# Optimization experiments

Measured on AMD Instinct MI355X. Metric: run time of the kernel, lower is better.

## Reference

```python
import jax, jax.numpy as jnp
import numpy as np

N_EMBD = 1024
N_HEAD = 16
HEAD_DIM = N_EMBD // N_HEAD
B, S = 4, 1024


def setup_inputs() -> dict:
    key = jax.random.key(0)
    k1, k2, k3 = jax.random.split(key, 3)
    scale = 0.02
    return {
        "x": jax.random.normal(k1, (B, S, N_EMBD), dtype=jnp.float32),
        "Wqkv": jax.random.normal(k2, (N_EMBD, 3 * N_EMBD), dtype=jnp.float32) * scale,
        "bqkv": jnp.zeros((3 * N_EMBD,), dtype=jnp.float32),
        "Wproj": jax.random.normal(k3, (N_EMBD, N_EMBD), dtype=jnp.float32) * scale,
        "bproj": jnp.zeros((N_EMBD,), dtype=jnp.float32),
    }


def reference(x, Wqkv, bqkv, Wproj, bproj):
    b, s, e = x.shape
    qkv = x @ Wqkv + bqkv  # (b, s, 3e)
    q, k, v = jnp.split(qkv, 3, axis=-1)
    # (b, h, s, d)
    q = q.reshape(b, s, N_HEAD, HEAD_DIM).transpose(0, 2, 1, 3)
    k = k.reshape(b, s, N_HEAD, HEAD_DIM).transpose(0, 2, 1, 3)
    v = v.reshape(b, s, N_HEAD, HEAD_DIM).transpose(0, 2, 1, 3)
    scores = jnp.einsum("bhqd,bhkd->bhqk", q, k) / jnp.sqrt(
        jnp.asarray(HEAD_DIM, dtype=x.dtype)
    )
    causal = jnp.tril(jnp.ones((s, s), dtype=bool))  # (s, s)
    scores = jnp.where(causal[None, None, :, :], scores, jnp.asarray(-jnp.inf, dtype=scores.dtype))
    attn = jax.nn.softmax(scores, axis=-1)
    out = jnp.einsum("bhqk,bhkd->bhqd", attn, v)
    out = out.transpose(0, 2, 1, 3).reshape(b, s, e)
    return out @ Wproj + bproj
```

## Files before the change

kernel.cpp:

```cpp
#include <hip/hip_runtime.h>

#define S_LEN 1024
#define EMB   1024
#define NH    16
#define HD    64
#define BATCH 4
#define M_TOT 4096
#define QSZ   (BATCH * NH * S_LEN * HD)

typedef __attribute__((ext_vector_type(4))) float  f32x4;
typedef __attribute__((ext_vector_type(8))) __bf16 bf16x8;

__device__ __forceinline__ unsigned short f2bf(float f) {
  union { float f; unsigned u; } a; a.f = f;
  unsigned r = a.u + 0x7fffu + ((a.u >> 16) & 1u);
  return (unsigned short)(r >> 16);
}

__device__ __forceinline__ float fexp2(float x) {
#if __has_builtin(__builtin_amdgcn_exp2f)
  return __builtin_amdgcn_exp2f(x);
#else
  return exp2f(x);
#endif
}

__global__ void cvt_bf16(const float4* __restrict__ in, ushort4* __restrict__ out, int n4) {
  int i = blockIdx.x * blockDim.x + threadIdx.x;
  if (i >= n4) return;
  float4 v = in[i];
  ushort4 o;
  o.x = f2bf(v.x); o.y = f2bf(v.y); o.z = f2bf(v.z); o.w = f2bf(v.w);
  out[i] = o;
}

__global__ void cvt_transpose(const float* __restrict__ in, unsigned short* __restrict__ out,
                              int K, int N) {
  __shared__ unsigned short tile[32][33];
  int n0 = blockIdx.x * 32, k0 = blockIdx.y * 32;
  int tx = threadIdx.x, ty = threadIdx.y;
  #pragma unroll
  for (int r = ty; r < 32; r += 8)
    tile[r][tx] = f2bf(in[(size_t)(k0 + r) * N + n0 + tx]);
  __syncthreads();
  #pragma unroll
  for (int r = ty; r < 32; r += 8)
    out[(size_t)(n0 + r) * K + k0 + tx] = tile[tx][r];
}

template<int EPI>
__global__ __launch_bounds__(256) void gemm_bt(
    const unsigned short* __restrict__ A,
    const unsigned short* __restrict__ Bt,
    const float* __restrict__ bias,
    void* __restrict__ outp,
    int M, int N, int K)
{
  __shared__ alignas(16) char smem[49152];
  unsigned short* As = (unsigned short*)smem;
  unsigned short* Bs = (unsigned short*)(smem + 24576);
  const int m0 = blockIdx.x * 128, n0 = blockIdx.y * 128;
  const int t = threadIdx.x;
  const int wid = t >> 6, lane = t & 63;
  const int wr = wid >> 1, wc = wid & 1;
  const int lr = lane & 15, lg = lane >> 4;
  const int nkt = K >> 5;

  f32x4 acc[4][4] = {};

  auto STAGE = [&](int b, int kt) {
    const int k0 = kt << 5;
    #pragma unroll
    for (int c = 0; c < 2; ++c) {
      int idx8 = (c * 4 + wid) * 64 + lane;
      int row  = idx8 >> 2, col = (idx8 & 3) << 3;
      const unsigned short* gA = A  + (size_t)(m0 + row) * K + k0 + col;
      const unsigned short* gB = Bt + (size_t)(n0 + row) * K + k0 + col;
      __builtin_amdgcn_global_load_lds(
          (const __attribute__((address_space(1))) unsigned int*)gA,
          (__attribute__((address_space(3))) unsigned int*)(As + b * 4096 + (c * 4 + wid) * 512),
          16, 0, 0);
      __builtin_amdgcn_global_load_lds(
          (const __attribute__((address_space(1))) unsigned int*)gB,
          (__attribute__((address_space(3))) unsigned int*)(Bs + b * 4096 + (c * 4 + wid) * 512),
          16, 0, 0);
    }
  };

  STAGE(0, 0);
  STAGE(1, 1);

  for (int kt = 0; kt < nkt; ++kt) {
    if (kt + 2 < nkt) {
      STAGE((kt + 2) % 3, kt + 2);
      asm volatile("s_waitcnt vmcnt(8)" ::: "memory");
    } else if (kt + 1 < nkt) {
      asm volatile("s_waitcnt vmcnt(4)" ::: "memory");
    } else {
      asm volatile("s_waitcnt vmcnt(0)" ::: "memory");
    }
    __builtin_amdgcn_s_barrier();
    asm volatile("" ::: "memory");

    const unsigned short* Ab = As + (kt % 3) * 4096;
    const unsigned short* Bb = Bs + (kt % 3) * 4096;
    bf16x8 af[4], bfr[4];
    #pragma unroll
    for (int i = 0; i < 4; ++i)
      af[i] = *(const bf16x8*)(Ab + (wr * 64 + i * 16 + lr) * 32 + lg * 8);
    #pragma unroll
    for (int j = 0; j < 4; ++j)
      bfr[j] = *(const bf16x8*)(Bb + (wc * 64 + j * 16 + lr) * 32 + lg * 8);
    __builtin_amdgcn_s_setprio(1);
    #pragma unroll
    for (int i = 0; i < 4; ++i)
      #pragma unroll
      for (int j = 0; j < 4; ++j)
        acc[i][j] = __builtin_amdgcn_mfma_f32_16x16x32_bf16(af[i], bfr[j], acc[i][j], 0, 0, 0);
    __builtin_amdgcn_s_setprio(0);

    asm volatile("s_waitcnt lgkmcnt(0)" ::: "memory");
    __builtin_amdgcn_s_barrier();
  }

  if (EPI == 0) {
    unsigned short* O = (unsigned short*)outp;
    const int sec = n0 >> 10;
    if (sec < 2) {
      #pragma unroll
      for (int i = 0; i < 4; ++i)
        #pragma unroll
        for (int j = 0; j < 4; ++j) {
          const int col = n0 + wc * 64 + j * 16 + lr;
          const float bv = bias[col];
          const int cc = col & 1023, h = cc >> 6, d = cc & 63;
          #pragma unroll
          for (int r = 0; r < 4; ++r) {
            const int row = m0 + wr * 64 + i * 16 + lg * 4 + r;
            float v = acc[i][j][r] + bv;
            if (sec == 0) v *= 0.18033688f;
            const int bb = row >> 10, ss = row & 1023;
            size_t off = (size_t)sec * QSZ +
                         (((size_t)(bb * NH + h) * S_LEN + ss) * HD + d);
            O[off] = f2bf(v);
          }
        }
    } else {
      unsigned short* T = (unsigned short*)smem;
      __syncthreads();
      #pragma unroll
      for (int i = 0; i < 4; ++i)
        #pragma unroll
        for (int j = 0; j < 4; ++j) {
          const int ci = wc * 64 + j * 16 + lr;
          const float bv = bias[n0 + ci];
          union { ushort4 s4; __bf16 b[4]; } pk;
          #pragma unroll
          for (int r = 0; r < 4; ++r) pk.b[r] = (__bf16)(acc[i][j][r] + bv);
          *(ushort4*)(T + ci * 136 + wr * 64 + i * 16 + lg * 4) = pk.s4;
        }
      __syncthreads();
      const int ci = t >> 1;
      const int cc = (n0 - 2048) + ci;
      const int h = cc >> 6, d = cc & 63;
      const int bb = m0 >> 10, s0 = m0 & 1023;
      unsigned short* dst = O + 2ull * QSZ +
          ((size_t)(bb * NH + h) * HD + d) * S_LEN + s0;
      #pragma unroll
      for (int q = 0; q < 8; ++q) {
        const int spos = (t & 1) * 8 + q;
        bf16x8 vv = *(const bf16x8*)(T + ci * 136 + spos * 8);
        *(bf16x8*)(dst + spos * 8) = vv;
      }
    }
  } else {
    #pragma unroll
    for (int i = 0; i < 4; ++i)
      #pragma unroll
      for (int j = 0; j < 4; ++j) {
        const int col = n0 + wc * 64 + j * 16 + lr;
        const float bv = bias[col];
        #pragma unroll
        for (int r = 0; r < 4; ++r) {
          const int row = m0 + wr * 64 + i * 16 + lg * 4 + r;
          ((float*)outp)[(size_t)row * (size_t)N + col] = acc[i][j][r] + bv;
        }
      }
  }
}

__device__ __forceinline__ void group_tile(
    const bf16x8 (&kf)[8], const bf16x8 (&vf)[8], const bf16x8 (&qf)[2],
    int kt, int q0, bool diag, int lr, int lg,
    float& m, float& lp, f32x4 (&o)[4])
{
  f32x4 sacc[4] = {};
  __builtin_amdgcn_s_setprio(1);
  #pragma unroll
  for (int nt = 0; nt < 4; ++nt)
    #pragma unroll
    for (int kk = 0; kk < 2; ++kk)
      sacc[nt] = __builtin_amdgcn_mfma_f32_16x16x32_bf16(kf[nt * 2 + kk], qf[kk], sacc[nt], 0, 0, 0);
  __builtin_amdgcn_s_setprio(0);

  float p[16];
  if (diag) {
    const int q = q0 + lr;
    #pragma unroll
    for (int nt = 0; nt < 4; ++nt)
      #pragma unroll
      for (int r = 0; r < 4; ++r) {
        int k = kt * 64 + nt * 16 + lg * 4 + r;
        p[nt * 4 + r] = (k > q) ? -1e30f : sacc[nt][r];
      }
  } else {
    #pragma unroll
    for (int nt = 0; nt < 4; ++nt)
      #pragma unroll
      for (int r = 0; r < 4; ++r)
        p[nt * 4 + r] = sacc[nt][r];
  }

  float r8[8], r4[4];
  #pragma unroll
  for (int i = 0; i < 8; ++i) r8[i] = fmaxf(p[i], p[i + 8]);
  #pragma unroll
  for (int i = 0; i < 4; ++i) r4[i] = fmaxf(r8[i], r8[i + 4]);
  float pm = fmaxf(fmaxf(r4[0], r4[1]), fmaxf(r4[2], r4[3]));
  if (__any(pm > m + 11.5f)) {
    float px = fmaxf(pm, __shfl_xor(pm, 16, 64));
    px = fmaxf(px, __shfl_xor(px, 32, 64));
    float mn = fmaxf(m, px);
    float fs = fexp2(m - mn);
    lp *= fs;
    #pragma unroll
    for (int dt = 0; dt < 4; ++dt)
      #pragma unroll
      for (int r = 0; r < 4; ++r) o[dt][r] *= fs;
    m = mn;
  }
  #pragma unroll
  for (int i = 0; i < 16; ++i) p[i] = fexp2(p[i] - m);

  float s8[8], s4[4];
  #pragma unroll
  for (int i = 0; i < 8; ++i) s8[i] = p[i] + p[i + 8];
  #pragma unroll
  for (int i = 0; i < 4; ++i) s4[i] = s8[i] + s8[i + 4];
  lp += (s4[0] + s4[1]) + (s4[2] + s4[3]);

  union { unsigned u[8]; __bf16 b[16]; } W;
  #pragma unroll
  for (int i = 0; i < 16; ++i) W.b[i] = (__bf16)p[i];

  const int dl0 = ((2 * (lg & 1) + (lg >> 1)) * 16 + lr) << 2;
  const int dl1 = ((2 * ((lg & 1) ^ 1) + (lg >> 1)) * 16 + lr) << 2;
  const bool oddlg = (lg & 1) != 0;
  const bool hb    = (lg >> 1) != 0;
  union { unsigned u[4]; bf16x8 v; } T0, T1;
  #pragma unroll
  for (int kk = 0; kk < 2; ++kk) {
    #pragma unroll
    for (int c = 0; c < 2; ++c) {
      unsigned vlo = W.u[4 * kk + c];
      unsigned vhi = W.u[4 * kk + 2 + c];
      unsigned s0 = oddlg ? vhi : vlo;
      unsigned s1 = oddlg ? vlo : vhi;
      unsigned r0 = (unsigned)__builtin_amdgcn_ds_permute(dl0, (int)s0);
      unsigned r1 = (unsigned)__builtin_amdgcn_ds_permute(dl1, (int)s1);
      unsigned* T = kk ? T1.u : T0.u;
      T[c]     = hb ? r1 : r0;
      T[2 + c] = hb ? r0 : r1;
    }
  }

  __builtin_amdgcn_s_setprio(1);
  #pragma unroll
  for (int dt = 0; dt < 4; ++dt) {
    o[dt] = __builtin_amdgcn_mfma_f32_16x16x32_bf16(vf[dt * 2 + 0], T0.v, o[dt], 0, 0, 0);
    o[dt] = __builtin_amdgcn_mfma_f32_16x16x32_bf16(vf[dt * 2 + 1], T1.v, o[dt], 0, 0, 0);
  }
  __builtin_amdgcn_s_setprio(0);
}

__device__ __forceinline__ void group_epilogue(
    const f32x4 (&o)[4], float lp, int q0, int lr, int lg,
    char* Ep, unsigned short* __restrict__ attout, int bb, int h)
{
  float l2 = lp + __shfl_xor(lp, 16, 64);
  float l4 = l2 + __shfl_xor(l2, 32, 64);
  float rl = 1.0f / l4;
  #pragma unroll
  for (int dt = 0; dt < 4; ++dt) {
    union { ushort4 s4; __bf16 b[4]; } ov;
    #pragma unroll
    for (int r = 0; r < 4; ++r) ov.b[r] = (__bf16)(o[dt][r] * rl);
    int byt = (lr * 128 + (dt * 16 + lg * 4) * 2) ^ ((lr & 7) << 4);
    *(ushort4*)(Ep + byt) = ov.s4;
  }
  asm volatile("s_waitcnt lgkmcnt(0)" ::: "memory");
  const int lane = lr + lg * 16;
  const int ql = lane >> 2, c = lane & 3;
  #pragma unroll
  for (int s = 0; s < 2; ++s) {
    int byt = (ql * 128 + (c * 16 + s * 8) * 2) ^ ((ql & 7) << 4);
    bf16x8 vrow = *(const bf16x8*)(Ep + byt);
    *(bf16x8*)(attout + (size_t)(bb * S_LEN + q0 + ql) * EMB + h * HD + c * 16 + s * 8) = vrow;
  }
}

__global__ __launch_bounds__(256, 2) void attn_fwd(
    const unsigned short* __restrict__ Q,
    const unsigned short* __restrict__ K,
    const unsigned short* __restrict__ Vt,
    unsigned short* __restrict__ attout)
{
  __shared__ alignas(16) char stage[2][16384];
  __shared__ alignas(16) char Ep_lds[4][2048];
  const int bid = blockIdx.x;
  const int bh   = ((bid & 7) << 3) | ((bid >> 3) & 7);
  const int base = bid >> 6;
  const int wv = threadIdx.x >> 6, lane = threadIdx.x & 63;
  const int pi = base * 4 + wv;
  const int lr = lane & 15, lg = lane >> 4;
  const int nkt  = 16 - base;
  const int nktl = base + 1;
  const int q0h = (63 - pi) * 16, q0l = pi * 16;
  const unsigned short* Qb = Q  + (size_t)bh * (S_LEN * HD);
  const unsigned short* Kh = K  + (size_t)bh * (S_LEN * HD);
  const unsigned short* Vh = Vt + (size_t)bh * (HD * S_LEN);
  const int bb = bh >> 4, h = bh & 15;

  auto STAGE = [&](int b, int kt) {
    char* lb = &stage[b][0];
    #pragma unroll
    for (int j = 0; j < 4; ++j) {
      if (wv < 2) {
        int L = wv * 4096 + j * 1024 + lane * 16;
        int row = L >> 7, c = (L >> 4) & 7;
        const unsigned short* src = Kh + (size_t)(kt * 64 + row) * HD + ((c ^ (row & 7)) << 3);
        __builtin_amdgcn_global_load_lds(
            (const __attribute__((address_space(1))) unsigned int*)src,
            (__attribute__((address_space(3))) unsigned int*)(lb + wv * 4096 + j * 1024),
            16, 0, 0);
      } else {
        int L = (wv - 2) * 4096 + j * 1024 + lane * 16;
        int row = L >> 7, c = (L >> 4) & 7;
        const unsigned short* src = Vh + (size_t)row * S_LEN + kt * 64 + ((c ^ (row & 7)) << 3);
        __builtin_amdgcn_global_load_lds(
            (const __attribute__((address_space(1))) unsigned int*)src,
            (__attribute__((address_space(3))) unsigned int*)(lb + 8192 + (wv - 2) * 4096 + j * 1024),
            16, 0, 0);
      }
    }
  };

  bf16x8 qfh[2], qfl[2];
  #pragma unroll
  for (int kk = 0; kk < 2; ++kk) {
    qfh[kk] = *(const bf16x8*)(Qb + (size_t)(q0h + lr) * HD + kk * 32 + lg * 8);
    qfl[kk] = *(const bf16x8*)(Qb + (size_t)(q0l + lr) * HD + kk * 32 + lg * 8);
  }

  float mh = -1e30f, lph = 0.f, ml = -1e30f, lpl = 0.f;
  f32x4 oh[4] = {}, ol[4] = {};

  STAGE(0, 0);
  asm volatile("s_waitcnt vmcnt(0)" ::: "memory");
  __syncthreads();

  for (int kt = 0; kt < nkt; ++kt) {
    const int cur = kt & 1;
    if (kt + 1 < nkt) STAGE(cur ^ 1, kt + 1);

    const char* sb = &stage[cur][0];
    bf16x8 kf[8], vf[8];
    #pragma unroll
    for (int nt = 0; nt < 4; ++nt)
      #pragma unroll
      for (int kk = 0; kk < 2; ++kk) {
        const int byt = (nt * 16 + lr) * 128 + ((((kk << 2) + lg) ^ (lr & 7)) << 4);
        kf[nt * 2 + kk] = *(const bf16x8*)(sb + byt);
        vf[nt * 2 + kk] = *(const bf16x8*)(sb + 8192 + byt);
      }

    group_tile(kf, vf, qfh, kt, q0h, kt == nkt - 1, lr, lg, mh, lph, oh);
    if (kt < nktl)
      group_tile(kf, vf, qfl, kt, q0l, kt == nktl - 1, lr, lg, ml, lpl, ol);

    asm volatile("s_waitcnt vmcnt(0)" ::: "memory");
    __syncthreads();
  }

  char* Ep = &Ep_lds[wv][0];
  group_epilogue(oh, lph, q0h, lr, lg, Ep, attout, bb, h);
  group_epilogue(ol, lpl, q0l, lr, lg, Ep, attout, bb, h);
}

extern "C" void kernel_launch(void* const* d_in, const int* in_sizes, int n_in,
                              void* d_out, int out_size, void* d_ws, size_t ws_size,
                              hipStream_t stream) {
  const float* x     = (const float*)d_in[0];
  const float* Wqkv  = (const float*)d_in[1];
  const float* bqkv  = (const float*)d_in[2];
  const float* Wproj = (const float*)d_in[3];
  const float* bproj = (const float*)d_in[4];

  unsigned short* xb     = (unsigned short*)d_ws;
  unsigned short* WqkvT  = xb     + (size_t)M_TOT * EMB;
  unsigned short* WprojT = WqkvT  + (size_t)3 * EMB * EMB;
  unsigned short* qkv    = WprojT + (size_t)EMB * EMB;
  unsigned short* att    = qkv    + 3ull * QSZ;

  cvt_bf16<<<dim3((M_TOT * EMB / 4 + 255) / 256), dim3(256), 0, stream>>>(
      (const float4*)x, (ushort4*)xb, M_TOT * EMB / 4);
  cvt_transpose<<<dim3(3 * EMB / 32, EMB / 32), dim3(32, 8), 0, stream>>>(Wqkv, WqkvT, EMB, 3 * EMB);
  cvt_transpose<<<dim3(EMB / 32, EMB / 32), dim3(32, 8), 0, stream>>>(Wproj, WprojT, EMB, EMB);

  gemm_bt<0><<<dim3(M_TOT / 128, 3 * EMB / 128), dim3(256), 0, stream>>>(
      xb, WqkvT, bqkv, (void*)qkv, M_TOT, 3 * EMB, EMB);

  attn_fwd<<<dim3(8 * BATCH * NH), dim3(256), 0, stream>>>(
      qkv, qkv + QSZ, qkv + 2ull * QSZ, att);

  gemm_bt<1><<<dim3(M_TOT / 128, EMB / 128), dim3(256), 0, stream>>>(
      att, WprojT, bproj, d_out, M_TOT, EMB, EMB);
}
```

Baseline: 99.92 us.

## Add 256x256-tile QKV GEMM with direct-to-LDS loads and swizzled shared memory

Replaces the generic 128x128 templated GEMM for the QKV projection with a dedicated 256x256-tile kernel. It uses 512 threads, a K step of 64, global_load_lds transfers straight into double-buffered LDS, and an XOR swizzle to avoid bank conflicts. The V-transpose epilogue is redone in four quadrant passes through shared memory. The aim is more operand reuse per block and cheaper staging, at the cost of only 192 blocks on the grid (fewer than the CU count) and 128 KB of LDS per block. The projection GEMM keeps the old design as a non-templated kernel.

```diff
diff --git a/kernel.cpp b/kernel.cpp
--- a/kernel.cpp
+++ b/kernel.cpp
@@ -48,12 +48,145 @@
     out[(size_t)(n0 + r) * K + k0 + tx] = tile[tx][r];
 }
 
-template<int EPI>
-__global__ __launch_bounds__(256) void gemm_bt(
+__global__ __launch_bounds__(512, 2) void gemm_qkv256(
     const unsigned short* __restrict__ A,
     const unsigned short* __restrict__ Bt,
     const float* __restrict__ bias,
-    void* __restrict__ outp,
+    unsigned short* __restrict__ O)
+{
+  __shared__ alignas(16) char smem[131072];
+  const int m0 = blockIdx.x * 256, n0 = blockIdx.y * 256;
+  const int K = EMB;
+  const int t = threadIdx.x;
+  const int wid = t >> 6, lane = t & 63;
+  const int wm = wid >> 2, wn = wid & 3;
+  const int lr = lane & 15, lg = lane >> 4;
+  const int nkt = K >> 6;
+
+  f32x4 acc[8][4] = {};
+
+  auto STAGE = [&](int b, int kt) {
+    const int k0 = kt << 6;
+    #pragma unroll
+    for (int l = 0; l < 4; ++l) {
+      const int L = l * 8192 + t * 16;
+      const int row = L >> 7;
+      const int c = (L >> 4) & 7;
+      const int ce = ((c ^ (row & 7)) << 3);
+      const unsigned short* gA = A  + (size_t)(m0 + row) * K + k0 + ce;
+      const unsigned short* gB = Bt + (size_t)(n0 + row) * K + k0 + ce;
+      __builtin_amdgcn_global_load_lds(
+          (const __attribute__((address_space(1))) unsigned int*)gA,
+          (__attribute__((address_space(3))) unsigned int*)(smem + b * 32768 + L),
+          16, 0, 0);
+      __builtin_amdgcn_global_load_lds(
+          (const __attribute__((address_space(1))) unsigned int*)gB,
+          (__attribute__((address_space(3))) unsigned int*)(smem + 65536 + b * 32768 + L),
+          16, 0, 0);
+    }
+  };
+
+  STAGE(0, 0);
+
+  for (int kt = 0; kt < nkt; ++kt) {
+    const int cur = kt & 1;
+    if (kt + 1 < nkt) {
+      STAGE(cur ^ 1, kt + 1);
+      asm volatile("s_waitcnt vmcnt(8)" ::: "memory");
+    } else {
+      asm volatile("s_waitcnt vmcnt(0)" ::: "memory");
+    }
+    __builtin_amdgcn_s_barrier();
+    asm volatile("" ::: "memory");
+
+    const char* Ab = smem + cur * 32768;
+    const char* Bb = smem + 65536 + cur * 32768;
+    #pragma unroll
+    for (int s = 0; s < 2; ++s) {
+      bf16x8 af[8], bfr[4];
+      #pragma unroll
+      for (int i = 0; i < 8; ++i) {
+        const int row = wm * 128 + i * 16 + lr;
+        const int byt = row * 128 + (((s * 4 + lg) ^ (row & 7)) << 4);
+        af[i] = *(const bf16x8*)(Ab + byt);
+      }
+      #pragma unroll
+      for (int j = 0; j < 4; ++j) {
+        const int row = wn * 64 + j * 16 + lr;
+        const int byt = row * 128 + (((s * 4 + lg) ^ (row & 7)) << 4);
+        bfr[j] = *(const bf16x8*)(Bb + byt);
+      }
+      __builtin_amdgcn_s_setprio(1);
+      #pragma unroll
+      for (int i = 0; i < 8; ++i)
+        #pragma unroll
+        for (int j = 0; j < 4; ++j)
+          acc[i][j] = __builtin_amdgcn_mfma_f32_16x16x32_bf16(af[i], bfr[j], acc[i][j], 0, 0, 0);
+      __builtin_amdgcn_s_setprio(0);
+    }
+    asm volatile("s_waitcnt lgkmcnt(0)" ::: "memory");
+    __builtin_amdgcn_s_barrier();
+  }
+
+  const int sec = n0 >> 10;
+  if (sec < 2) {
+    #pragma unroll
+    for (int i = 0; i < 8; ++i)
+      #pragma unroll
+      for (int j = 0; j < 4; ++j) {
+        const int col = n0 + wn * 64 + j * 16 + lr;
+        const float bv = bias[col];
+        const int cc = col & 1023, h = cc >> 6, d = cc & 63;
+        #pragma unroll
+        for (int r = 0; r < 4; ++r) {
+          const int row = m0 + wm * 128 + i * 16 + lg * 4 + r;
+          float v = acc[i][j][r] + bv;
+          if (sec == 0) v *= 0.18033688f;
+          const int bb = row >> 10, ss = row & 1023;
+          O[(size_t)sec * QSZ + (((size_t)(bb * NH + h) * S_LEN + ss) * HD + d)] = f2bf(v);
+        }
+      }
+  } else {
+    unsigned short* T = (unsigned short*)smem;
+    const int bb2 = m0 >> 10, sbase = m0 & 1023;
+    #pragma unroll
+    for (int qr = 0; qr < 2; ++qr)
+      #pragma unroll
+      for (int qc = 0; qc < 2; ++qc) {
+        __syncthreads();
+        if (wm == qr && (wn >> 1) == qc) {
+          #pragma unroll
+          for (int i = 0; i < 8; ++i)
+            #pragma unroll
+            for (int j = 0; j < 4; ++j) {
+              const int ci = (wn & 1) * 64 + j * 16 + lr;
+              const float bv = bias[n0 + qc * 128 + ci];
+              union { ushort4 s4; __bf16 b[4]; } pk;
+              #pragma unroll
+              for (int r = 0; r < 4; ++r) pk.b[r] = (__bf16)(acc[i][j][r] + bv);
+              *(ushort4*)(T + ci * 136 + i * 16 + lg * 4) = pk.s4;
+            }
+        }
+        __syncthreads();
+        const int ci = t >> 2, part = t & 3;
+        const int cc = (n0 - 2048) + qc * 128 + ci;
+        const int h = cc >> 6, d = cc & 63;
+        unsigned short* dst = O + 2ull * QSZ +
+            ((size_t)(bb2 * NH + h) * HD + d) * S_LEN + sbase + qr * 128;
+        #pragma unroll
+        for (int u = 0; u < 4; ++u) {
+          const int spos = part * 32 + u * 8;
+          *(bf16x8*)(dst + spos) = *(const bf16x8*)(T + ci * 136 + spos);
+        }
+      }
+  }
+}
+
+__global__ __launch_bounds__(256) void gemm_proj(
+    const unsigned short* __restrict__ A,
+    const unsigned short* __restrict__ Bt,
+    const float* __restrict__ bias,
+    float* __restrict__ outp,
     int M, int N, int K)
 {
   __shared__ alignas(16) char smem[49152];
@@ -123,70 +256,18 @@
     __builtin_amdgcn_s_barrier();
   }
 
-  if (EPI == 0) {
-    unsigned short* O = (unsigned short*)outp;
-    const int sec = n0 >> 10;
-    if (sec < 2) {
-      #pragma unroll
-      for (int i = 0; i < 4; ++i)
-        #pragma unroll
-        for (int j = 0; j < 4; ++j) {
-          const int col = n0 + wc * 64 + j * 16 + lr;
-          const float bv = bias[col];
-          const int cc = col & 1023, h = cc >> 6, d = cc & 63;
-          #pragma unroll
-          for (int r = 0; r < 4; ++r) {
-            const int row = m0 + wr * 64 + i * 16 + lg * 4 + r;
-            float v = acc[i][j][r] + bv;
-            if (sec == 0) v *= 0.18033688f;
-            const int bb = row >> 10, ss = row & 1023;
-            size_t off = (size_t)sec * QSZ +
-                         (((size_t)(bb * NH + h) * S_LEN + ss) * HD + d);
-            O[off] = f2bf(v);
-          }
-        }
-    } else {
-      unsigned short* T = (unsigned short*)smem;
-      __syncthreads();
-      #pragma unroll
-      for (int i = 0; i < 4; ++i)
-        #pragma unroll
-        for (int j = 0; j < 4; ++j) {
-          const int ci = wc * 64 + j * 16 + lr;
-          const float bv = bias[n0 + ci];
-          union { ushort4 s4; __bf16 b[4]; } pk;
-          #pragma unroll
-          for (int r = 0; r < 4; ++r) pk.b[r] = (__bf16)(acc[i][j][r] + bv);
-          *(ushort4*)(T + ci * 136 + wr * 64 + i * 16 + lg * 4) = pk.s4;
-        }
-      __syncthreads();
-      const int ci = t >> 1;
-      const int cc = (n0 - 2048) + ci;
-      const int h = cc >> 6, d = cc & 63;
-      const int bb = m0 >> 10, s0 = m0 & 1023;
-      unsigned short* dst = O + 2ull * QSZ +
-          ((size_t)(bb * NH + h) * HD + d) * S_LEN + s0;
-      #pragma unroll
-      for (int q = 0; q < 8; ++q) {
-        const int spos = (t & 1) * 8 + q;
-        bf16x8 vv = *(const bf16x8*)(T + ci * 136 + spos * 8);
-        *(bf16x8*)(dst + spos * 8) = vv;
-      }
-    }
-  } else {
-    #pragma unroll
-    for (int i = 0; i < 4; ++i)
-      #pragma unroll
-      for (int j = 0; j < 4; ++j) {
-        const int col = n0 + wc * 64 + j * 16 + lr;
-        const float bv = bias[col];
-        #pragma unroll
-        for (int r = 0; r < 4; ++r) {
-          const int row = m0 + wr * 64 + i * 16 + lg * 4 + r;
-          ((float*)outp)[(size_t)row * (size_t)N + col] = acc[i][j][r] + bv;
-        }
-      }
-  }
+  #pragma unroll
+  for (int i = 0; i < 4; ++i)
+    #pragma unroll
+    for (int j = 0; j < 4; ++j) {
+      const int col = n0 + wc * 64 + j * 16 + lr;
+      const float bv = bias[col];
+      #pragma unroll
+      for (int r = 0; r < 4; ++r) {
+        const int row = m0 + wr * 64 + i * 16 + lg * 4 + r;
+        outp[(size_t)row * (size_t)N + col] = acc[i][j][r] + bv;
+      }
+    }
 }
 
 __device__ __forceinline__ void group_tile(
@@ -417,12 +498,12 @@
   cvt_transpose<<<dim3(3 * EMB / 32, EMB / 32), dim3(32, 8), 0, stream>>>(Wqkv, WqkvT, EMB, 3 * EMB);
   cvt_transpose<<<dim3(EMB / 32, EMB / 32), dim3(32, 8), 0, stream>>>(Wproj, WprojT, EMB, EMB);
 
-  gemm_bt<0><<<dim3(M_TOT / 128, 3 * EMB / 128), dim3(256), 0, stream>>>(
-      xb, WqkvT, bqkv, (void*)qkv, M_TOT, 3 * EMB, EMB);
+  gemm_qkv256<<<dim3(M_TOT / 256, 3 * EMB / 256), dim3(512), 0, stream>>>(
+      xb, WqkvT, bqkv, qkv);
 
   attn_fwd<<<dim3(8 * BATCH * NH), dim3(256), 0, stream>>>(
       qkv, qkv + QSZ, qkv + 2ull * QSZ, att);
 
-  gemm_bt<1><<<dim3(M_TOT / 128, EMB / 128), dim3(256), 0, stream>>>(
-      att, WprojT, bproj, d_out, M_TOT, EMB, EMB);
-}
+  gemm_proj<<<dim3(M_TOT / 128, EMB / 128), dim3(256), 0, stream>>>(
+      att, WprojT, bproj, (float*)d_out, M_TOT, EMB, EMB);
+}
```

New measurement: 98.67 us. No clear change (-1.3%).

## Restructure GEMM to 8-wave blocks with BK=64 double buffering and swizzled LDS

Applied to the files above, without the earlier changes.

The bf16 GEMM kernel now uses 512 threads (8 waves, each computing a 64x32 sub-tile) instead of 256 threads. The K-tile grows from 32 to 64, and the pipeline goes from a 3-stage to a 2-stage LDS buffer. Global-to-LDS staging and fragment reads use an XOR swizzle on 16-byte chunks to avoid LDS bank conflicts. The intent is more latency hiding and fewer conflicts, but the launch_bounds(512,4) hint may cap registers tightly enough to cause spills, and the shallower pipeline offers less prefetch depth.

```diff
diff --git a/kernel.cpp b/kernel.cpp
--- a/kernel.cpp
+++ b/kernel.cpp
@@ -49,52 +49,49 @@
 }
 
 template<int EPI>
-__global__ __launch_bounds__(256) void gemm_bt(
+__global__ __launch_bounds__(512, 4) void gemm_tile(
     const unsigned short* __restrict__ A,
     const unsigned short* __restrict__ Bt,
     const float* __restrict__ bias,
     void* __restrict__ outp,
-    int M, int N, int K)
+    int K, int Nout)
 {
-  __shared__ alignas(16) char smem[49152];
-  unsigned short* As = (unsigned short*)smem;
-  unsigned short* Bs = (unsigned short*)(smem + 24576);
+  __shared__ alignas(16) char smem[65536];
   const int m0 = blockIdx.x * 128, n0 = blockIdx.y * 128;
   const int t = threadIdx.x;
   const int wid = t >> 6, lane = t & 63;
-  const int wr = wid >> 1, wc = wid & 1;
+  const int wm = wid >> 2, wn = wid & 3;
   const int lr = lane & 15, lg = lane >> 4;
-  const int nkt = K >> 5;
-
-  f32x4 acc[4][4] = {};
+  const int nkt = K >> 6;
+
+  f32x4 acc[4][2] = {};
 
   auto STAGE = [&](int b, int kt) {
-    const int k0 = kt << 5;
-    #pragma unroll
-    for (int c = 0; c < 2; ++c) {
-      int idx8 = (c * 4 + wid) * 64 + lane;
-      int row  = idx8 >> 2, col = (idx8 & 3) << 3;
-      const unsigned short* gA = A  + (size_t)(m0 + row) * K + k0 + col;
-      const unsigned short* gB = Bt + (size_t)(n0 + row) * K + k0 + col;
+    const int k0 = kt << 6;
+    #pragma unroll
+    for (int l = 0; l < 2; ++l) {
+      const int L = l * 8192 + t * 16;
+      const int row = L >> 7, c = (L >> 4) & 7;
+      const int ce = (c ^ (row & 7)) << 3;
+      const unsigned short* gA = A  + (size_t)(m0 + row) * K + k0 + ce;
+      const unsigned short* gB = Bt + (size_t)(n0 + row) * K + k0 + ce;
       __builtin_amdgcn_global_load_lds(
           (const __attribute__((address_space(1))) unsigned int*)gA,
-          (__attribute__((address_space(3))) unsigned int*)(As + b * 4096 + (c * 4 + wid) * 512),
+          (__attribute__((address_space(3))) unsigned int*)(smem + b * 32768 + L),
           16, 0, 0);
       __builtin_amdgcn_global_load_lds(
           (const __attribute__((address_space(1))) unsigned int*)gB,
-          (__attribute__((address_space(3))) unsigned int*)(Bs + b * 4096 + (c * 4 + wid) * 512),
+          (__attribute__((address_space(3))) unsigned int*)(smem + b * 32768 + 16384 + L),
           16, 0, 0);
     }
   };
 
   STAGE(0, 0);
-  STAGE(1, 1);
 
   for (int kt = 0; kt < nkt; ++kt) {
-    if (kt + 2 < nkt) {
-      STAGE((kt + 2) % 3, kt + 2);
-      asm volatile("s_waitcnt vmcnt(8)" ::: "memory");
-    } else if (kt + 1 < nkt) {
+    const int cur = kt & 1;
+    if (kt + 1 < nkt) {
+      STAGE(cur ^ 1, kt + 1);
       asm volatile("s_waitcnt vmcnt(4)" ::: "memory");
     } else {
       asm volatile("s_waitcnt vmcnt(0)" ::: "memory");
@@ -102,21 +99,31 @@
     __builtin_amdgcn_s_barrier();
     asm volatile("" ::: "memory");
 
-    const unsigned short* Ab = As + (kt % 3) * 4096;
-    const unsigned short* Bb = Bs + (kt % 3) * 4096;
-    bf16x8 af[4], bfr[4];
+    const char* Ab = smem + cur * 32768;
+    const char* Bb = Ab + 16384;
+    bf16x8 af[4][2], bfr[2][2];
     #pragma unroll
     for (int i = 0; i < 4; ++i)
-      af[i] = *(const bf16x8*)(Ab + (wr * 64 + i * 16 + lr) * 32 + lg * 8);
-    #pragma unroll
-    for (int j = 0; j < 4; ++j)
-      bfr[j] = *(const bf16x8*)(Bb + (wc * 64 + j * 16 + lr) * 32 + lg * 8);
+      #pragma unroll
+      for (int kk = 0; kk < 2; ++kk) {
+        const int row = wm * 64 + i * 16 + lr;
+        af[i][kk] = *(const bf16x8*)(Ab + row * 128 + (((kk * 4 + lg) ^ (row & 7)) << 4));
+      }
+    #pragma unroll
+    for (int j = 0; j < 2; ++j)
+      #pragma unroll
+      for (int kk = 0; kk < 2; ++kk) {
+        const int row = wn * 32 + j * 16 + lr;
+        bfr[j][kk] = *(const bf16x8*)(Bb + row * 128 + (((kk * 4 + lg) ^ (row & 7)) << 4));
+      }
     __builtin_amdgcn_s_setprio(1);
     #pragma unroll
     for (int i = 0; i < 4; ++i)
       #pragma unroll
-      for (int j = 0; j < 4; ++j)
-        acc[i][j] = __builtin_amdgcn_mfma_f32_16x16x32_bf16(af[i], bfr[j], acc[i][j], 0, 0, 0);
+      for (int j = 0; j < 2; ++j)
+        #pragma unroll
+        for (int kk = 0; kk < 2; ++kk)
+          acc[i][j] = __builtin_amdgcn_mfma_f32_16x16x32_bf16(af[i][kk], bfr[j][kk], acc[i][j], 0, 0, 0);
     __builtin_amdgcn_s_setprio(0);
 
     asm volatile("s_waitcnt lgkmcnt(0)" ::: "memory");
@@ -130,60 +137,57 @@
       #pragma unroll
       for (int i = 0; i < 4; ++i)
         #pragma unroll
-        for (int j = 0; j < 4; ++j) {
-          const int col = n0 + wc * 64 + j * 16 + lr;
+        for (int j = 0; j < 2; ++j) {
+          const int col = n0 + wn * 32 + j * 16 + lr;
           const float bv = bias[col];
           const int cc = col & 1023, h = cc >> 6, d = cc & 63;
           #pragma unroll
           for (int r = 0; r < 4; ++r) {
-            const int row = m0 + wr * 64 + i * 16 + lg * 4 + r;
+            const int row = m0 + wm * 64 + i * 16 + lg * 4 + r;
             float v = acc[i][j][r] + bv;
             if (sec == 0) v *= 0.18033688f;
             const int bb = row >> 10, ss = row & 1023;
-            size_t off = (size_t)sec * QSZ +
-                         (((size_t)(bb * NH + h) * S_LEN + ss) * HD + d);
-            O[off] = f2bf(v);
+            O[(size_t)sec * QSZ + (((size_t)(bb * NH + h) * S_LEN + ss) * HD + d)] = f2bf(v);
           }
         }
     } else {
       unsigned short* T = (unsigned short*)smem;
-      __syncthreads();
       #pragma unroll
       for (int i = 0; i < 4; ++i)
         #pragma unroll
-        for (int j = 0; j < 4; ++j) {
-          const int ci = wc * 64 + j * 16 + lr;
+        for (int j = 0; j < 2; ++j) {
+          const int ci = wn * 32 + j * 16 + lr;
           const float bv = bias[n0 + ci];
           union { ushort4 s4; __bf16 b[4]; } pk;
           #pragma unroll
           for (int r = 0; r < 4; ++r) pk.b[r] = (__bf16)(acc[i][j][r] + bv);
-          *(ushort4*)(T + ci * 136 + wr * 64 + i * 16 + lg * 4) = pk.s4;
+          *(ushort4*)(T + ci * 136 + wm * 64 + i * 16 + lg * 4) = pk.s4;
         }
       __syncthreads();
-      const int ci = t >> 1;
+      const int ci = t >> 2, part = t & 3;
       const int cc = (n0 - 2048) + ci;
       const int h = cc >> 6, d = cc & 63;
-      const int bb = m0 >> 10, s0 = m0 & 1023;
+      const int bb2 = m0 >> 10, sbase = m0 & 1023;
       unsigned short* dst = O + 2ull * QSZ +
-          ((size_t)(bb * NH + h) * HD + d) * S_LEN + s0;
-      #pragma unroll
-      for (int q = 0; q < 8; ++q) {
-        const int spos = (t & 1) * 8 + q;
-        bf16x8 vv = *(const bf16x8*)(T + ci * 136 + spos * 8);
-        *(bf16x8*)(dst + spos * 8) = vv;
+          ((size_t)(bb2 * NH + h) * HD + d) * S_LEN + sbase;
+      #pragma unroll
+      for (int u = 0; u < 4; ++u) {
+        const int spos = part * 32 + u * 8;
+        *(bf16x8*)(dst + spos) = *(const bf16x8*)(T + ci * 136 + spos);
       }
     }
   } else {
+    float* Of = (float*)outp;
     #pragma unroll
     for (int i = 0; i < 4; ++i)
       #pragma unroll
-      for (int j = 0; j < 4; ++j) {
-        const int col = n0 + wc * 64 + j * 16 + lr;
+      for (int j = 0; j < 2; ++j) {
+        const int col = n0 + wn * 32 + j * 16 + lr;
         const float bv = bias[col];
         #pragma unroll
         for (int r = 0; r < 4; ++r) {
-          const int row = m0 + wr * 64 + i * 16 + lg * 4 + r;
-          ((float*)outp)[(size_t)row * (size_t)N + col] = acc[i][j][r] + bv;
+          const int row = m0 + wm * 64 + i * 16 + lg * 4 + r;
+          Of[(size_t)row * (size_t)Nout + col] = acc[i][j][r] + bv;
         }
       }
   }
@@ -417,12 +421,12 @@
   cvt_transpose<<<dim3(3 * EMB / 32, EMB / 32), dim3(32, 8), 0, stream>>>(Wqkv, WqkvT, EMB, 3 * EMB);
   cvt_transpose<<<dim3(EMB / 32, EMB / 32), dim3(32, 8), 0, stream>>>(Wproj, WprojT, EMB, EMB);
 
-  gemm_bt<0><<<dim3(M_TOT / 128, 3 * EMB / 128), dim3(256), 0, stream>>>(
-      xb, WqkvT, bqkv, (void*)qkv, M_TOT, 3 * EMB, EMB);
+  gemm_tile<0><<<dim3(M_TOT / 128, 3 * EMB / 128), dim3(512), 0, stream>>>(
+      xb, WqkvT, bqkv, (void*)qkv, EMB, 0);
 
   attn_fwd<<<dim3(8 * BATCH * NH), dim3(256), 0, stream>>>(
       qkv, qkv + QSZ, qkv + 2ull * QSZ, att);
 
-  gemm_bt<1><<<dim3(M_TOT / 128, EMB / 128), dim3(256), 0, stream>>>(
-      att, WprojT, bproj, d_out, M_TOT, EMB, EMB);
-}
+  gemm_tile<1><<<dim3(M_TOT / 128, EMB / 128), dim3(512), 0, stream>>>(
+      att, WprojT, bproj, d_out, EMB, EMB);
+}
```

Result: faster. 91.32 us (-8.6%).
